# Kernel tuning notes

Hardware: AMD Instinct MI355X
Metric: run time of the kernel (lower is better)

The kernel has to match this reference:

```python
import jax, jax.numpy as jnp
import numpy as np

N_NODES = 1_000_000
F_IN = 128
F_OUT = 128
K = 10
B = 16384
U1 = B * (K + 1)  # 1-hop frontier size (batch + sampled neighbors, dedup skipped)


def relu6(x):
    return jnp.clip(x, 0.0, 6.0)


def setup_inputs() -> dict:
    key = jax.random.key(0)
    k1, k2, k3, k4, k5, k6, k7 = jax.random.split(key, 7)
    raw_features = jax.random.normal(k1, (N_NODES, F_IN), dtype=jnp.float32)
    # xavier-ish scale for [out, 2*in] weights
    W1 = jax.random.normal(k2, (F_OUT, 2 * F_IN), dtype=jnp.float32) * 0.05
    W2 = jax.random.normal(k3, (F_OUT, 2 * F_OUT), dtype=jnp.float32) * 0.05
    u1_global = jax.random.randint(k4, (U1,), 0, N_NODES)
    neigh1_global = jax.random.randint(k5, (U1, K), 0, N_NODES)
    self2_local = jax.random.randint(k6, (B,), 0, U1)
    neigh2_local = jax.random.randint(k7, (B, K), 0, U1)
    return {
        "raw_features": raw_features,
        "W1": W1,
        "W2": W2,
        "u1_global": u1_global,
        "neigh1_global": neigh1_global,
        "self2_local": self2_local,
        "neigh2_local": neigh2_local,
    }


def _sage_layer(self_feats, agg_feats, W):
    # combined = cat([self, agg]); out = relu6(W @ combined.T).T
    combined = jnp.concatenate([self_feats, agg_feats], axis=1)
    return relu6(combined @ W.T)


def reference(raw_features, W1, W2, u1_global, neigh1_global, self2_local, neigh2_local):
    # Layer 1: aggregate raw features over sampled global neighbors (MEAN == row-normalized mask.mm)
    agg1 = jnp.mean(raw_features[neigh1_global], axis=1)  # [U1, F_IN]
    agg1 = jnp.where(jnp.isnan(agg1), jnp.float32(0.5), agg1)
    h1 = _sage_layer(raw_features[u1_global], agg1, W1)  # [U1, F_OUT]
    # Layer 2: aggregate layer-1 embeddings over frontier-local neighbor indices
    agg2 = jnp.mean(h1[neigh2_local], axis=1)  # [B, F_OUT]
    agg2 = jnp.where(jnp.isnan(agg2), jnp.float32(0.5), agg2)
    h2 = _sage_layer(h1[self2_local], agg2, W2)  # [B, F_OUT]
    return h2
```

## Files before the change

### kernel.cpp

```cpp
#include <hip/hip_runtime.h>
#include <hip/hip_bf16.h>
#include <math.h>


#define F    128
#define KNB  10
#define BM   32

__global__ __launch_bounds__(256) void transpose_w(const float* __restrict__ W,
                                                   float* __restrict__ WT) {
    int e = blockIdx.x * 256 + threadIdx.x;
    int o = e >> 8;
    int j = e & 255;
    WT[j * F + o] = W[e];
}

__global__ __launch_bounds__(256) void sage_layer(
    const float* __restrict__ feats,
    const float* __restrict__ WT,
    const int*   __restrict__ selfIdx,
    const int*   __restrict__ neighIdx,
    float*       __restrict__ out,
    int nrows)
{
    __shared__ float Xs[BM][68];
    __shared__ float Ws[64][132];
    __shared__ int   sidx[BM];
    __shared__ int   nidx[BM * KNB];

    const int t  = threadIdx.x;
    const int r0 = blockIdx.x * BM;

    if (t < BM)             sidx[t]       = selfIdx[r0 + t];
    if (t < BM * KNB)       nidx[t]       = neighIdx[(size_t)r0 * KNB + t];
    if (t + 256 < BM * KNB) nidx[t + 256] = neighIdx[(size_t)r0 * KNB + t + 256];

    const int ct = (t >> 6) * 8 + (t & 7);
    const int rt = (t >> 3) & 7;

    const int grow = t >> 4;
    const int gc4  = t & 15;

    float4 acc[4];
    #pragma unroll
    for (int i = 0; i < 4; ++i) acc[i] = make_float4(0.f, 0.f, 0.f, 0.f);

    for (int kk = 0; kk < 4; ++kk) {
        __syncthreads();

        {
            const float4* src = (const float4*)(WT + (size_t)kk * 64 * F);
            #pragma unroll
            for (int it = 0; it < 8; ++it) {
                int e4 = t + it * 256;
                int jj = e4 >> 5;
                int o4 = e4 & 31;
                *(float4*)&Ws[jj][o4 * 4] = src[e4];
            }
        }

        if (kk < 2) {
            #pragma unroll
            for (int half = 0; half < 2; ++half) {
                int row = grow + half * 16;
                const float4* src =
                    (const float4*)(feats + (size_t)sidx[row] * F + kk * 64);
                *(float4*)&Xs[row][gc4 * 4] = src[gc4];
            }
        } else {
            #pragma unroll
            for (int half = 0; half < 2; ++half) {
                int row = grow + half * 16;
                float4 a = make_float4(0.f, 0.f, 0.f, 0.f);
                #pragma unroll
                for (int k = 0; k < KNB; ++k) {
                    const float4* src = (const float4*)(
                        feats + (size_t)nidx[row * KNB + k] * F + (kk - 2) * 64);
                    float4 v = src[gc4];
                    a.x += v.x; a.y += v.y; a.z += v.z; a.w += v.w;
                }
                const float inv = 1.0f / (float)KNB;
                a.x *= inv; a.y *= inv; a.z *= inv; a.w *= inv;
                if (isnan(a.x)) a.x = 0.5f;
                if (isnan(a.y)) a.y = 0.5f;
                if (isnan(a.z)) a.z = 0.5f;
                if (isnan(a.w)) a.w = 0.5f;
                *(float4*)&Xs[row][gc4 * 4] = a;
            }
        }
        __syncthreads();

        #pragma unroll
        for (int jj = 0; jj < 64; jj += 4) {
            float4 xv[4], wv[4];
            #pragma unroll
            for (int i = 0; i < 4; ++i)
                xv[i] = *(const float4*)&Xs[rt + 8 * i][jj];
            #pragma unroll
            for (int q = 0; q < 4; ++q)
                wv[q] = *(const float4*)&Ws[jj + q][ct * 4];
            #pragma unroll
            for (int i = 0; i < 4; ++i) {
                acc[i].x += xv[i].x * wv[0].x + xv[i].y * wv[1].x
                          + xv[i].z * wv[2].x + xv[i].w * wv[3].x;
                acc[i].y += xv[i].x * wv[0].y + xv[i].y * wv[1].y
                          + xv[i].z * wv[2].y + xv[i].w * wv[3].y;
                acc[i].z += xv[i].x * wv[0].z + xv[i].y * wv[1].z
                          + xv[i].z * wv[2].z + xv[i].w * wv[3].z;
                acc[i].w += xv[i].x * wv[0].w + xv[i].y * wv[1].w
                          + xv[i].z * wv[2].w + xv[i].w * wv[3].w;
            }
        }
    }

    #pragma unroll
    for (int i = 0; i < 4; ++i) {
        int r = r0 + rt + 8 * i;
        float4 v = acc[i];
        v.x = fminf(fmaxf(v.x, 0.f), 6.f);
        v.y = fminf(fmaxf(v.y, 0.f), 6.f);
        v.z = fminf(fmaxf(v.z, 0.f), 6.f);
        v.w = fminf(fmaxf(v.w, 0.f), 6.f);
        *(float4*)&out[(size_t)r * F + ct * 4] = v;
    }
}

extern "C" void kernel_launch(void* const* d_in, const int* in_sizes, int n_in,
                              void* d_out, int out_size, void* d_ws, size_t ws_size,
                              hipStream_t stream) {
    const float* raw = (const float*)d_in[0];
    const float* W1  = (const float*)d_in[1];
    const float* W2  = (const float*)d_in[2];
    const int*   u1  = (const int*)d_in[3];
    const int*   n1  = (const int*)d_in[4];
    const int*   s2  = (const int*)d_in[5];
    const int*   n2  = (const int*)d_in[6];
    float* out = (float*)d_out;

    const int U1n = in_sizes[3];
    const int Bn  = in_sizes[5];

    float* ws  = (float*)d_ws;
    float* WT1 = ws;
    float* WT2 = ws + 256 * 128;
    float* h1  = ws + 2 * 256 * 128;

    hipLaunchKernelGGL(transpose_w, dim3(128), dim3(256), 0, stream, W1, WT1);
    hipLaunchKernelGGL(transpose_w, dim3(128), dim3(256), 0, stream, W2, WT2);

    hipLaunchKernelGGL(sage_layer, dim3(U1n / BM), dim3(256), 0, stream,
                       raw, WT1, u1, n1, h1, U1n);
    hipLaunchKernelGGL(sage_layer, dim3(Bn / BM), dim3(256), 0, stream,
                       h1, WT2, s2, n2, out, Bn);
}
```

Before: 1.056 ms.

## Split neighbor gather-mean into separate kernel before dense SAGE matmul

Moves the neighbor mean aggregation out of the fused GEMM kernel into a standalone gather kernel. That kernel issues all ten row loads per warp at once so more memory requests are in flight, and writes the aggregated features to workspace. The dense kernel then reads them contiguously. This adds a full write and read of a U1×128 intermediate plus extra launches, and falls back to the fused path if the workspace is too small.

```diff
diff --git a/kernel.cpp b/kernel.cpp
--- a/kernel.cpp
+++ b/kernel.cpp
@@ -15,7 +15,144 @@
     WT[j * F + o] = W[e];
 }
 
-__global__ __launch_bounds__(256) void sage_layer(
+__global__ __launch_bounds__(256) void gather_mean(
+    const float* __restrict__ feats,
+    const int*   __restrict__ neighIdx,
+    float*       __restrict__ agg,
+    int nrows)
+{
+    const int t    = threadIdx.x;
+    const int row  = blockIdx.x * 8 + (t >> 5);
+    const int lane = t & 31;
+    if (row >= nrows) return;
+
+    const int* nb = neighIdx + (size_t)row * KNB;
+    int n0 = nb[0], n1 = nb[1], n2 = nb[2], n3 = nb[3], n4 = nb[4];
+    int n5 = nb[5], n6 = nb[6], n7 = nb[7], n8 = nb[8], n9 = nb[9];
+
+    const size_t c = (size_t)lane * 4;
+    float4 v0 = *(const float4*)(feats + (size_t)n0 * F + c);
+    float4 v1 = *(const float4*)(feats + (size_t)n1 * F + c);
+    float4 v2 = *(const float4*)(feats + (size_t)n2 * F + c);
+    float4 v3 = *(const float4*)(feats + (size_t)n3 * F + c);
+    float4 v4 = *(const float4*)(feats + (size_t)n4 * F + c);
+    float4 v5 = *(const float4*)(feats + (size_t)n5 * F + c);
+    float4 v6 = *(const float4*)(feats + (size_t)n6 * F + c);
+    float4 v7 = *(const float4*)(feats + (size_t)n7 * F + c);
+    float4 v8 = *(const float4*)(feats + (size_t)n8 * F + c);
+    float4 v9 = *(const float4*)(feats + (size_t)n9 * F + c);
+
+    float4 s;
+    s.x = ((v0.x + v1.x) + (v2.x + v3.x)) + ((v4.x + v5.x) + (v6.x + v7.x)) + (v8.x + v9.x);
+    s.y = ((v0.y + v1.y) + (v2.y + v3.y)) + ((v4.y + v5.y) + (v6.y + v7.y)) + (v8.y + v9.y);
+    s.z = ((v0.z + v1.z) + (v2.z + v3.z)) + ((v4.z + v5.z) + (v6.z + v7.z)) + (v8.z + v9.z);
+    s.w = ((v0.w + v1.w) + (v2.w + v3.w)) + ((v4.w + v5.w) + (v6.w + v7.w)) + (v8.w + v9.w);
+    const float inv = 1.0f / (float)KNB;
+    s.x *= inv; s.y *= inv; s.z *= inv; s.w *= inv;
+    if (isnan(s.x)) s.x = 0.5f;
+    if (isnan(s.y)) s.y = 0.5f;
+    if (isnan(s.z)) s.z = 0.5f;
+    if (isnan(s.w)) s.w = 0.5f;
+
+    *(float4*)(agg + (size_t)row * F + c) = s;
+}
+
+__global__ __launch_bounds__(256) void sage_dense(
+    const float* __restrict__ feats,
+    const float* __restrict__ agg,
+    const float* __restrict__ WT,
+    const int*   __restrict__ selfIdx,
+    float*       __restrict__ out,
+    int nrows)
+{
+    __shared__ float Xs[BM][68];
+    __shared__ float Ws[64][132];
+    __shared__ int   sidx[BM];
+
+    const int t  = threadIdx.x;
+    const int r0 = blockIdx.x * BM;
+
+    if (t < BM) sidx[t] = selfIdx[r0 + t];
+
+    const int ct = (t >> 6) * 8 + (t & 7);
+    const int rt = (t >> 3) & 7;
+
+    const int grow = t >> 4;
+    const int gc4  = t & 15;
+
+    float4 acc[4];
+    #pragma unroll
+    for (int i = 0; i < 4; ++i) acc[i] = make_float4(0.f, 0.f, 0.f, 0.f);
+
+    for (int kk = 0; kk < 4; ++kk) {
+        __syncthreads();
+
+        {
+            const float4* src = (const float4*)(WT + (size_t)kk * 64 * F);
+            #pragma unroll
+            for (int it = 0; it < 8; ++it) {
+                int e4 = t + it * 256;
+                int jj = e4 >> 5;
+                int o4 = e4 & 31;
+                *(float4*)&Ws[jj][o4 * 4] = src[e4];
+            }
+        }
+
+        if (kk < 2) {
+            #pragma unroll
+            for (int half = 0; half < 2; ++half) {
+                int row = grow + half * 16;
+                const float4* src =
+                    (const float4*)(feats + (size_t)sidx[row] * F + kk * 64);
+                *(float4*)&Xs[row][gc4 * 4] = src[gc4];
+            }
+        } else {
+            #pragma unroll
+            for (int half = 0; half < 2; ++half) {
+                int row = grow + half * 16;
+                const float4* src =
+                    (const float4*)(agg + (size_t)(r0 + row) * F + (kk - 2) * 64);
+                *(float4*)&Xs[row][gc4 * 4] = src[gc4];
+            }
+        }
+        __syncthreads();
+
+        #pragma unroll
+        for (int jj = 0; jj < 64; jj += 4) {
+            float4 xv[4], wv[4];
+            #pragma unroll
+            for (int i = 0; i < 4; ++i)
+                xv[i] = *(const float4*)&Xs[rt + 8 * i][jj];
+            #pragma unroll
+            for (int q = 0; q < 4; ++q)
+                wv[q] = *(const float4*)&Ws[jj + q][ct * 4];
+            #pragma unroll
+            for (int i = 0; i < 4; ++i) {
+                acc[i].x += xv[i].x * wv[0].x + xv[i].y * wv[1].x
+                          + xv[i].z * wv[2].x + xv[i].w * wv[3].x;
+                acc[i].y += xv[i].x * wv[0].y + xv[i].y * wv[1].y
+                          + xv[i].z * wv[2].y + xv[i].w * wv[3].y;
+                acc[i].z += xv[i].x * wv[0].z + xv[i].y * wv[1].z
+                          + xv[i].z * wv[2].z + xv[i].w * wv[3].z;
+                acc[i].w += xv[i].x * wv[0].w + xv[i].y * wv[1].w
+                          + xv[i].z * wv[2].w + xv[i].w * wv[3].w;
+            }
+        }
+    }
+
+    #pragma unroll
+    for (int i = 0; i < 4; ++i) {
+        int r = r0 + rt + 8 * i;
+        float4 v = acc[i];
+        v.x = fminf(fmaxf(v.x, 0.f), 6.f);
+        v.y = fminf(fmaxf(v.y, 0.f), 6.f);
+        v.z = fminf(fmaxf(v.z, 0.f), 6.f);
+        v.w = fminf(fmaxf(v.w, 0.f), 6.f);
+        *(float4*)&out[(size_t)r * F + ct * 4] = v;
+    }
+}
+
+__global__ __launch_bounds__(256) void sage_fused(
     const float* __restrict__ feats,
     const float* __restrict__ WT,
     const int*   __restrict__ selfIdx,
@@ -37,7 +174,6 @@
 
     const int ct = (t >> 6) * 8 + (t & 7);
     const int rt = (t >> 3) & 7;
-
     const int grow = t >> 4;
     const int gc4  = t & 15;
 
@@ -47,7 +183,6 @@
 
     for (int kk = 0; kk < 4; ++kk) {
         __syncthreads();
-
         {
             const float4* src = (const float4*)(WT + (size_t)kk * 64 * F);
             #pragma unroll
@@ -58,7 +193,6 @@
                 *(float4*)&Ws[jj][o4 * 4] = src[e4];
             }
         }
-
         if (kk < 2) {
             #pragma unroll
             for (int half = 0; half < 2; ++half) {
@@ -142,14 +276,30 @@
 
     float* ws  = (float*)d_ws;
     float* WT1 = ws;
-    float* WT2 = ws + 256 * 128;
-    float* h1  = ws + 2 * 256 * 128;
+    float* WT2 = WT1 + 256 * 128;
+    float* h1  = WT2 + 256 * 128;
+    float* ag1 = h1  + (size_t)U1n * F;
+    float* ag2 = ag1 + (size_t)U1n * F;
+
+    const size_t need = ((size_t)2 * 256 * 128 + (size_t)U1n * F * 2 + (size_t)Bn * F)
+                        * sizeof(float);
 
     hipLaunchKernelGGL(transpose_w, dim3(128), dim3(256), 0, stream, W1, WT1);
     hipLaunchKernelGGL(transpose_w, dim3(128), dim3(256), 0, stream, W2, WT2);
 
-    hipLaunchKernelGGL(sage_layer, dim3(U1n / BM), dim3(256), 0, stream,
-                       raw, WT1, u1, n1, h1, U1n);
-    hipLaunchKernelGGL(sage_layer, dim3(Bn / BM), dim3(256), 0, stream,
-                       h1, WT2, s2, n2, out, Bn);
-}
+    if (ws_size >= need) {
+        hipLaunchKernelGGL(gather_mean, dim3(U1n / 8), dim3(256), 0, stream,
+                           raw, n1, ag1, U1n);
+        hipLaunchKernelGGL(sage_dense, dim3(U1n / BM), dim3(256), 0, stream,
+                           raw, ag1, WT1, u1, h1, U1n);
+        hipLaunchKernelGGL(gather_mean, dim3(Bn / 8), dim3(256), 0, stream,
+                           h1, n2, ag2, Bn);
+        hipLaunchKernelGGL(sage_dense, dim3(Bn / BM), dim3(256), 0, stream,
+                           h1, ag2, WT2, s2, out, Bn);
+    } else {
+        hipLaunchKernelGGL(sage_fused, dim3(U1n / BM), dim3(256), 0, stream,
+                           raw, WT1, u1, n1, h1, U1n);
+        hipLaunchKernelGGL(sage_fused, dim3(Bn / BM), dim3(256), 0, stream,
+                           h1, WT2, s2, n2, out, Bn);
+    }
+}
```

Result: slower. 1.133 ms (+7.2%).

## Split neighbor mean-gather into its own kernel and enlarge dense GEMM tile

Applied to the files above, without the earlier changes.

Moves the 10-neighbor mean aggregation out of the fused layer into a separate gather kernel that processes one row per 32-lane group and writes the aggregate to workspace. The dense kernel then reads self rows and the precomputed aggregate into a larger tile of 128 rows, with each thread computing 8x8 outputs. This reuses each weight tile across more rows and gives the gather more memory parallelism. In exchange it adds an extra round trip of the aggregate through global memory and two more kernel launches.

```diff
diff --git a/kernel.cpp b/kernel.cpp
--- a/kernel.cpp
+++ b/kernel.cpp
@@ -5,7 +5,7 @@
 
 #define F    128
 #define KNB  10
-#define BM   32
+#define BM   128
 
 __global__ __launch_bounds__(256) void transpose_w(const float* __restrict__ W,
                                                    float* __restrict__ WT) {
@@ -15,35 +15,77 @@
     WT[j * F + o] = W[e];
 }
 
-__global__ __launch_bounds__(256) void sage_layer(
+__global__ __launch_bounds__(256) void gather_mean(
     const float* __restrict__ feats,
+    const int*   __restrict__ neighIdx,
+    float*       __restrict__ agg,
+    int nrows)
+{
+    const int t    = threadIdx.x;
+    const int row  = blockIdx.x * 8 + (t >> 5);
+    const int lane = t & 31;
+    if (row >= nrows) return;
+
+    const int* nb = neighIdx + (size_t)row * KNB;
+    int n0 = nb[0], n1 = nb[1], n2 = nb[2], n3 = nb[3], n4 = nb[4];
+    int n5 = nb[5], n6 = nb[6], n7 = nb[7], n8 = nb[8], n9 = nb[9];
+
+    const size_t c = (size_t)lane * 4;
+    float4 v0 = *(const float4*)(feats + (size_t)n0 * F + c);
+    float4 v1 = *(const float4*)(feats + (size_t)n1 * F + c);
+    float4 v2 = *(const float4*)(feats + (size_t)n2 * F + c);
+    float4 v3 = *(const float4*)(feats + (size_t)n3 * F + c);
+    float4 v4 = *(const float4*)(feats + (size_t)n4 * F + c);
+    float4 v5 = *(const float4*)(feats + (size_t)n5 * F + c);
+    float4 v6 = *(const float4*)(feats + (size_t)n6 * F + c);
+    float4 v7 = *(const float4*)(feats + (size_t)n7 * F + c);
+    float4 v8 = *(const float4*)(feats + (size_t)n8 * F + c);
+    float4 v9 = *(const float4*)(feats + (size_t)n9 * F + c);
+
+    float4 s;
+    s.x = ((v0.x + v1.x) + (v2.x + v3.x)) + ((v4.x + v5.x) + (v6.x + v7.x)) + (v8.x + v9.x);
+    s.y = ((v0.y + v1.y) + (v2.y + v3.y)) + ((v4.y + v5.y) + (v6.y + v7.y)) + (v8.y + v9.y);
+    s.z = ((v0.z + v1.z) + (v2.z + v3.z)) + ((v4.z + v5.z) + (v6.z + v7.z)) + (v8.z + v9.z);
+    s.w = ((v0.w + v1.w) + (v2.w + v3.w)) + ((v4.w + v5.w) + (v6.w + v7.w)) + (v8.w + v9.w);
+    const float inv = 1.0f / (float)KNB;
+    s.x *= inv; s.y *= inv; s.z *= inv; s.w *= inv;
+    if (isnan(s.x)) s.x = 0.5f;
+    if (isnan(s.y)) s.y = 0.5f;
+    if (isnan(s.z)) s.z = 0.5f;
+    if (isnan(s.w)) s.w = 0.5f;
+
+    *(float4*)(agg + (size_t)row * F + c) = s;
+}
+
+__global__ __launch_bounds__(256, 2) void sage_dense(
+    const float* __restrict__ feats,
+    const float* __restrict__ agg,
     const float* __restrict__ WT,
     const int*   __restrict__ selfIdx,
-    const int*   __restrict__ neighIdx,
     float*       __restrict__ out,
     int nrows)
 {
     __shared__ float Xs[BM][68];
     __shared__ float Ws[64][132];
     __shared__ int   sidx[BM];
-    __shared__ int   nidx[BM * KNB];
 
     const int t  = threadIdx.x;
     const int r0 = blockIdx.x * BM;
 
-    if (t < BM)             sidx[t]       = selfIdx[r0 + t];
-    if (t < BM * KNB)       nidx[t]       = neighIdx[(size_t)r0 * KNB + t];
-    if (t + 256 < BM * KNB) nidx[t + 256] = neighIdx[(size_t)r0 * KNB + t + 256];
-
-    const int ct = (t >> 6) * 8 + (t & 7);
-    const int rt = (t >> 3) & 7;
+    if (t < BM) sidx[t] = selfIdx[r0 + t];
+
+    const int ctg = t & 15;
+    const int rt  = t >> 4;
 
     const int grow = t >> 4;
     const int gc4  = t & 15;
 
-    float4 acc[4];
+    float4 accA[8], accB[8];
     #pragma unroll
-    for (int i = 0; i < 4; ++i) acc[i] = make_float4(0.f, 0.f, 0.f, 0.f);
+    for (int i = 0; i < 8; ++i) {
+        accA[i] = make_float4(0.f, 0.f, 0.f, 0.f);
+        accB[i] = make_float4(0.f, 0.f, 0.f, 0.f);
+    }
 
     for (int kk = 0; kk < 4; ++kk) {
         __syncthreads();
@@ -61,67 +103,71 @@
 
         if (kk < 2) {
             #pragma unroll
-            for (int half = 0; half < 2; ++half) {
-                int row = grow + half * 16;
+            for (int it = 0; it < 8; ++it) {
+                int row = grow + it * 16;
                 const float4* src =
                     (const float4*)(feats + (size_t)sidx[row] * F + kk * 64);
                 *(float4*)&Xs[row][gc4 * 4] = src[gc4];
             }
         } else {
             #pragma unroll
-            for (int half = 0; half < 2; ++half) {
-                int row = grow + half * 16;
-                float4 a = make_float4(0.f, 0.f, 0.f, 0.f);
-                #pragma unroll
-                for (int k = 0; k < KNB; ++k) {
-                    const float4* src = (const float4*)(
-                        feats + (size_t)nidx[row * KNB + k] * F + (kk - 2) * 64);
-                    float4 v = src[gc4];
-                    a.x += v.x; a.y += v.y; a.z += v.z; a.w += v.w;
-                }
-                const float inv = 1.0f / (float)KNB;
-                a.x *= inv; a.y *= inv; a.z *= inv; a.w *= inv;
-                if (isnan(a.x)) a.x = 0.5f;
-                if (isnan(a.y)) a.y = 0.5f;
-                if (isnan(a.z)) a.z = 0.5f;
-                if (isnan(a.w)) a.w = 0.5f;
-                *(float4*)&Xs[row][gc4 * 4] = a;
+            for (int it = 0; it < 8; ++it) {
+                int row = grow + it * 16;
+                const float4* src =
+                    (const float4*)(agg + (size_t)(r0 + row) * F + (kk - 2) * 64);
+                *(float4*)&Xs[row][gc4 * 4] = src[gc4];
             }
         }
         __syncthreads();
 
-        #pragma unroll
+        #pragma unroll 8
         for (int jj = 0; jj < 64; jj += 4) {
-            float4 xv[4], wv[4];
-            #pragma unroll
-            for (int i = 0; i < 4; ++i)
-                xv[i] = *(const float4*)&Xs[rt + 8 * i][jj];
-            #pragma unroll
-            for (int q = 0; q < 4; ++q)
-                wv[q] = *(const float4*)&Ws[jj + q][ct * 4];
-            #pragma unroll
-            for (int i = 0; i < 4; ++i) {
-                acc[i].x += xv[i].x * wv[0].x + xv[i].y * wv[1].x
-                          + xv[i].z * wv[2].x + xv[i].w * wv[3].x;
-                acc[i].y += xv[i].x * wv[0].y + xv[i].y * wv[1].y
-                          + xv[i].z * wv[2].y + xv[i].w * wv[3].y;
-                acc[i].z += xv[i].x * wv[0].z + xv[i].y * wv[1].z
-                          + xv[i].z * wv[2].z + xv[i].w * wv[3].z;
-                acc[i].w += xv[i].x * wv[0].w + xv[i].y * wv[1].w
-                          + xv[i].z * wv[2].w + xv[i].w * wv[3].w;
+            float4 xv[8], wA[4], wB[4];
+            #pragma unroll
+            for (int q = 0; q < 4; ++q) {
+                wA[q] = *(const float4*)&Ws[jj + q][ctg * 4];
+                wB[q] = *(const float4*)&Ws[jj + q][ctg * 4 + 64];
+            }
+            #pragma unroll
+            for (int i = 0; i < 8; ++i)
+                xv[i] = *(const float4*)&Xs[rt + 16 * i][jj];
+            #pragma unroll
+            for (int i = 0; i < 8; ++i) {
+                accA[i].x += xv[i].x * wA[0].x + xv[i].y * wA[1].x
+                           + xv[i].z * wA[2].x + xv[i].w * wA[3].x;
+                accA[i].y += xv[i].x * wA[0].y + xv[i].y * wA[1].y
+                           + xv[i].z * wA[2].y + xv[i].w * wA[3].y;
+                accA[i].z += xv[i].x * wA[0].z + xv[i].y * wA[1].z
+                           + xv[i].z * wA[2].z + xv[i].w * wA[3].z;
+                accA[i].w += xv[i].x * wA[0].w + xv[i].y * wA[1].w
+                           + xv[i].z * wA[2].w + xv[i].w * wA[3].w;
+                accB[i].x += xv[i].x * wB[0].x + xv[i].y * wB[1].x
+                           + xv[i].z * wB[2].x + xv[i].w * wB[3].x;
+                accB[i].y += xv[i].x * wB[0].y + xv[i].y * wB[1].y
+                           + xv[i].z * wB[2].y + xv[i].w * wB[3].y;
+                accB[i].z += xv[i].x * wB[0].z + xv[i].y * wB[1].z
+                           + xv[i].z * wB[2].z + xv[i].w * wB[3].z;
+                accB[i].w += xv[i].x * wB[0].w + xv[i].y * wB[1].w
+                           + xv[i].z * wB[2].w + xv[i].w * wB[3].w;
             }
         }
     }
 
     #pragma unroll
-    for (int i = 0; i < 4; ++i) {
-        int r = r0 + rt + 8 * i;
-        float4 v = acc[i];
+    for (int i = 0; i < 8; ++i) {
+        int r = r0 + rt + 16 * i;
+        float4 v = accA[i];
         v.x = fminf(fmaxf(v.x, 0.f), 6.f);
         v.y = fminf(fmaxf(v.y, 0.f), 6.f);
         v.z = fminf(fmaxf(v.z, 0.f), 6.f);
         v.w = fminf(fmaxf(v.w, 0.f), 6.f);
-        *(float4*)&out[(size_t)r * F + ct * 4] = v;
+        *(float4*)&out[(size_t)r * F + ctg * 4] = v;
+        float4 u = accB[i];
+        u.x = fminf(fmaxf(u.x, 0.f), 6.f);
+        u.y = fminf(fmaxf(u.y, 0.f), 6.f);
+        u.z = fminf(fmaxf(u.z, 0.f), 6.f);
+        u.w = fminf(fmaxf(u.w, 0.f), 6.f);
+        *(float4*)&out[(size_t)r * F + ctg * 4 + 64] = u;
     }
 }
 
@@ -142,14 +188,20 @@
 
     float* ws  = (float*)d_ws;
     float* WT1 = ws;
-    float* WT2 = ws + 256 * 128;
-    float* h1  = ws + 2 * 256 * 128;
+    float* WT2 = WT1 + 256 * 128;
+    float* h1  = WT2 + 256 * 128;
+    float* ag1 = h1  + (size_t)U1n * F;
+    float* ag2 = ag1 + (size_t)U1n * F;
 
     hipLaunchKernelGGL(transpose_w, dim3(128), dim3(256), 0, stream, W1, WT1);
     hipLaunchKernelGGL(transpose_w, dim3(128), dim3(256), 0, stream, W2, WT2);
 
-    hipLaunchKernelGGL(sage_layer, dim3(U1n / BM), dim3(256), 0, stream,
-                       raw, WT1, u1, n1, h1, U1n);
-    hipLaunchKernelGGL(sage_layer, dim3(Bn / BM), dim3(256), 0, stream,
-                       h1, WT2, s2, n2, out, Bn);
-}
+    hipLaunchKernelGGL(gather_mean, dim3(U1n / 8), dim3(256), 0, stream,
+                       raw, n1, ag1, U1n);
+    hipLaunchKernelGGL(sage_dense, dim3(U1n / BM), dim3(256), 0, stream,
+                       raw, ag1, WT1, u1, h1, U1n);
+    hipLaunchKernelGGL(gather_mean, dim3(Bn / 8), dim3(256), 0, stream,
+                       h1, n2, ag2, Bn);
+    hipLaunchKernelGGL(sage_dense, dim3(Bn / BM), dim3(256), 0, stream,
+                       h1, ag2, WT2, s2, out, Bn);
+}
```

Result: faster. 936.5 us (-11.3%).
